# Optimization experiments

Measured on AMD Instinct MI355X. Metric: run time of the kernel, lower is better.

## Reference

```python
import jax, jax.numpy as jnp
import numpy as np

B, NQ, NK, D, H = 4, 512, 512, 128, 32  # batch, n_queries, n_keys, kq_size, mlp hidden


def setup_inputs() -> dict:
    key = jax.random.key(0)
    ks = jax.random.split(key, 7)
    s_in = 1.0 / np.sqrt(2 * D)
    s_h = 1.0 / np.sqrt(H)
    return {
        "keys": jax.random.normal(ks[0], (B, NK, D), dtype=jnp.float32),
        "queries": jax.random.normal(ks[1], (B, NQ, D), dtype=jnp.float32),
        # first MLP layer Linear(2D, H) split into key-half and query-half
        "Wk": jax.random.uniform(ks[2], (D, H), jnp.float32, -s_in, s_in),
        "Wq": jax.random.uniform(ks[3], (D, H), jnp.float32, -s_in, s_in),
        "b1": jax.random.uniform(ks[4], (H,), jnp.float32, -s_in, s_in),
        # second MLP layer Linear(H, 1)
        "w2": jax.random.uniform(ks[5], (H,), jnp.float32, -s_h, s_h),
        "b2": jax.random.uniform(ks[6], (), jnp.float32, -s_h, s_h),
    }


def reference(keys, queries, Wk, Wq, b1, w2, b2):
    # AdditiveScorer: logits[b,q,k] = w2 . tanh(W1 @ [keys[b,k]; queries[b,q]] + b1) + b2
    # Split the concat-linear into two GEMMs (identical math, no [B,Q,K,2D] tensor).
    kh = jnp.einsum("bkd,dh->bkh", keys, Wk)            # (B, NK, H)
    qh = jnp.einsum("bqd,dh->bqh", queries, Wq)          # (B, NQ, H)
    h = jnp.tanh(qh[:, :, None, :] + kh[:, None, :, :] + b1)  # (B, NQ, NK, H)
    logits = jnp.einsum("bqkh,h->bqk", h, w2) + b2       # (B, NQ, NK)
    attn = jax.nn.softmax(logits, axis=-1)               # softmax over keys
    context = jnp.einsum("bqk,bkd->bqd", attn, keys)     # weighted value sum (values = keys)
    return context
```

## Files before the change

### kernel.cpp

```cpp
#include <hip/hip_runtime.h>

#define B 4
#define NQ 512
#define NK 512
#define D 128
#define H 32
#define G 4
#define PS 2.8853900817779268f

__device__ __forceinline__ float rcp_f(float x)  { return __builtin_amdgcn_rcpf(x); }
__device__ __forceinline__ float exp2_f(float x) { return __builtin_amdgcn_exp2f(x); }

__device__ __forceinline__ void fma4(float4& a, const float4& v, float s) {
    a.x = fmaf(s, v.x, a.x);
    a.y = fmaf(s, v.y, a.y);
    a.z = fmaf(s, v.z, a.z);
    a.w = fmaf(s, v.w, a.w);
}

__global__ __launch_bounds__(256) void proj_kernel(
    const float* __restrict__ keys, const float* __restrict__ queries,
    const float* __restrict__ Wk, const float* __restrict__ Wq,
    const float* __restrict__ b1,
    float* __restrict__ Ek, float* __restrict__ eq)
{
    __shared__ float xs[8][D];
    const int tid = threadIdx.x;
    const int r0 = blockIdx.x * 8;
    const bool is_q = (r0 >= B * NK);
    const float* __restrict__ X = is_q ? (queries + (size_t)(r0 - B * NK) * D)
                                       : (keys + (size_t)r0 * D);
    const float* __restrict__ W = is_q ? Wq : Wk;

    reinterpret_cast<float4*>(&xs[0][0])[tid] =
        reinterpret_cast<const float4*>(X)[tid];
    __syncthreads();

    const int lr = tid >> 5;
    const int h  = tid & 31;
    float a0 = 0.f, a1 = 0.f, a2 = 0.f, a3 = 0.f;
    const float4* x4 = reinterpret_cast<const float4*>(&xs[lr][0]);
    #pragma unroll
    for (int i = 0; i < D / 4; ++i) {
        float4 v = x4[i];
        a0 = fmaf(v.x, W[(4 * i + 0) * H + h], a0);
        a1 = fmaf(v.y, W[(4 * i + 1) * H + h], a1);
        a2 = fmaf(v.z, W[(4 * i + 2) * H + h], a2);
        a3 = fmaf(v.w, W[(4 * i + 3) * H + h], a3);
    }
    float acc = (a0 + a1) + (a2 + a3);
    if (is_q) {
        const int rq = r0 - B * NK + lr;
        eq[(size_t)rq * H + h] = exp2_f(acc * PS);
    } else {
        const int r = r0 + lr;
        const int b = r >> 9;
        const int k = r & (NK - 1);
        Ek[((size_t)b * H + h) * NK + k] = exp2_f((acc + b1[h]) * PS);
    }
}

__global__ __launch_bounds__(512) void attend_kernel(
    const float* __restrict__ keys,
    const float* __restrict__ Ek,
    const float* __restrict__ eq,
    const float* __restrict__ w2,
    float* __restrict__ outp)
{
    __shared__ float lp[8][256];
    __shared__ float ex_t[G][NK];
    __shared__ float acc_s[16][G][D];
    __shared__ float eq_s[G][H];
    __shared__ float w2_s[H];

    const int tid  = threadIdx.x;
    const int lane = tid & 63;
    const int w    = tid >> 6;
    const int qw   = w & 3;
    const int half = w >> 2;
    const int b    = blockIdx.x >> 7;
    const int q0   = (blockIdx.x & 127) * G;

    if (lane < H) {
        if (w < 4)  eq_s[w][lane] = eq[((size_t)b * NQ + q0 + w) * H + lane];
        if (w == 4) w2_s[lane] = -PS * w2[lane];
    }
    __syncthreads();

    float l0 = 0.f, l1 = 0.f, l2 = 0.f, l3 = 0.f;
    const float* Ekb = Ek + (size_t)b * H * NK + half * 256;
    #pragma unroll 8
    for (int h = 0; h < H; ++h) {
        const float4 v = reinterpret_cast<const float4*>(Ekb + h * NK)[lane];
        const float ev = eq_s[qw][h];
        const float wp = w2_s[h];
        l0 = fmaf(wp, rcp_f(fmaf(ev, v.x, 1.f)), l0);
        l1 = fmaf(wp, rcp_f(fmaf(ev, v.y, 1.f)), l1);
        l2 = fmaf(wp, rcp_f(fmaf(ev, v.z, 1.f)), l2);
        l3 = fmaf(wp, rcp_f(fmaf(ev, v.w, 1.f)), l3);
    }
    {
        const float4 st = { l0, l1, l2, l3 };
        reinterpret_cast<float4*>(&lp[w][0])[lane] = st;
    }
    __syncthreads();

    if (w < 4) {
        float l[8];
        {
            const float4 L0 = reinterpret_cast<const float4*>(&lp[w][0])[lane];
            const float4 L1 = reinterpret_cast<const float4*>(&lp[w + 4][0])[lane];
            l[0] = L0.x; l[1] = L0.y; l[2] = L0.z; l[3] = L0.w;
            l[4] = L1.x; l[5] = L1.y; l[6] = L1.z; l[7] = L1.w;
        }
        float m = l[0];
        #pragma unroll
        for (int j = 1; j < 8; ++j) m = fmaxf(m, l[j]);
        #pragma unroll
        for (int off = 32; off; off >>= 1) m = fmaxf(m, __shfl_xor(m, off));
        float e[8], s = 0.f;
        #pragma unroll
        for (int j = 0; j < 8; ++j) { e[j] = exp2_f(l[j] - m); s += e[j]; }
        #pragma unroll
        for (int off = 32; off; off >>= 1) s += __shfl_xor(s, off);
        const float inv = 1.f / s;
        const float4 st0 = { e[0] * inv, e[1] * inv, e[2] * inv, e[3] * inv };
        const float4 st1 = { e[4] * inv, e[5] * inv, e[6] * inv, e[7] * inv };
        reinterpret_cast<float4*>(&ex_t[w][0])[lane]   = st0;
        reinterpret_cast<float4*>(&ex_t[w][256])[lane] = st1;
    }
    __syncthreads();

    const int dg = tid & 31;
    const int kp = tid >> 5;
    const float4* k4 = reinterpret_cast<const float4*>(
        keys + ((size_t)b * NK + kp * 32) * D) + dg;
    const float4* e0p = reinterpret_cast<const float4*>(&ex_t[0][kp * 32]);
    const float4* e1p = reinterpret_cast<const float4*>(&ex_t[1][kp * 32]);
    const float4* e2p = reinterpret_cast<const float4*>(&ex_t[2][kp * 32]);
    const float4* e3p = reinterpret_cast<const float4*>(&ex_t[3][kp * 32]);
    float4 a0 = {0,0,0,0}, a1 = a0, a2 = a0, a3 = a0;
    #pragma unroll 2
    for (int kk4 = 0; kk4 < 8; ++kk4) {
        float ea[4], eb[4], ec[4], ed[4];
        *reinterpret_cast<float4*>(ea) = e0p[kk4];
        *reinterpret_cast<float4*>(eb) = e1p[kk4];
        *reinterpret_cast<float4*>(ec) = e2p[kk4];
        *reinterpret_cast<float4*>(ed) = e3p[kk4];
        #pragma unroll
        for (int j = 0; j < 4; ++j) {
            float4 kv = k4[(size_t)(4 * kk4 + j) * (D / 4)];
            fma4(a0, kv, ea[j]);
            fma4(a1, kv, eb[j]);
            fma4(a2, kv, ec[j]);
            fma4(a3, kv, ed[j]);
        }
    }
    *reinterpret_cast<float4*>(&acc_s[kp][0][4 * dg]) = a0;
    *reinterpret_cast<float4*>(&acc_s[kp][1][4 * dg]) = a1;
    *reinterpret_cast<float4*>(&acc_s[kp][2][4 * dg]) = a2;
    *reinterpret_cast<float4*>(&acc_s[kp][3][4 * dg]) = a3;
    __syncthreads();

    const int g = tid >> 7;
    const int d = tid & 127;
    float r = 0.f;
    #pragma unroll
    for (int p = 0; p < 16; ++p) r += acc_s[p][g][d];
    outp[((size_t)b * NQ + q0 + g) * D + d] = r;
}

extern "C" void kernel_launch(void* const* d_in, const int* in_sizes, int n_in,
                              void* d_out, int out_size, void* d_ws, size_t ws_size,
                              hipStream_t stream) {
    const float* keys    = (const float*)d_in[0];
    const float* queries = (const float*)d_in[1];
    const float* Wk      = (const float*)d_in[2];
    const float* Wq      = (const float*)d_in[3];
    const float* b1      = (const float*)d_in[4];
    const float* w2      = (const float*)d_in[5];
    float* out = (float*)d_out;

    float* Ek = (float*)d_ws;
    float* eq = Ek + (size_t)B * H * NK;

    const int proj_blocks = (B * NK + B * NQ) / 8;
    proj_kernel<<<proj_blocks, 256, 0, stream>>>(keys, queries, Wk, Wq, b1, Ek, eq);
    attend_kernel<<<B * NQ / G, 512, 0, stream>>>(keys, Ek, eq, w2, out);
}
```

Baseline: 20.24 us.

## Process eight queries per block with LDS-staged key projections and packed FMA

The attend kernel now handles eight queries per block instead of four, so each block stages the batch's full exp-key projection slab (64KB) in LDS once and reuses it across all eight query waves. Each wave now scores a single query over all 512 keys, which removes the cross-wave logit merge and the max subtraction in the softmax. The scoring loop uses v_pk_fma_f32 on packed pairs. The value-sum phase keeps eight accumulators per thread, which doubles reuse of each loaded key. In exchange there are half as many blocks, much more LDS per block (about 82KB dynamic), higher register pressure, and a softmax without max subtraction that depends on logits staying bounded.

```diff
diff --git a/kernel.cpp b/kernel.cpp
--- a/kernel.cpp
+++ b/kernel.cpp
@@ -5,11 +5,19 @@
 #define NK 512
 #define D 128
 #define H 32
-#define G 4
+#define G 8
 #define PS 2.8853900817779268f
+
+typedef float f32x2 __attribute__((ext_vector_type(2)));
 
 __device__ __forceinline__ float rcp_f(float x)  { return __builtin_amdgcn_rcpf(x); }
 __device__ __forceinline__ float exp2_f(float x) { return __builtin_amdgcn_exp2f(x); }
+
+__device__ __forceinline__ f32x2 pk_fma(f32x2 a, f32x2 b, f32x2 c) {
+    f32x2 d;
+    asm("v_pk_fma_f32 %0, %1, %2, %3" : "=v"(d) : "v"(a), "v"(b), "v"(c));
+    return d;
+}
 
 __device__ __forceinline__ void fma4(float4& a, const float4& v, float s) {
     a.x = fmaf(s, v.x, a.x);
@@ -67,107 +75,128 @@
     const float* __restrict__ w2,
     float* __restrict__ outp)
 {
-    __shared__ float lp[8][256];
-    __shared__ float ex_t[G][NK];
-    __shared__ float acc_s[16][G][D];
-    __shared__ float eq_s[G][H];
-    __shared__ float w2_s[H];
+    extern __shared__ float smem[];
+    float* slab = smem;
+    float* exw  = smem + H * NK;
+    float* eqw  = smem + H * NK + G * NK;
 
     const int tid  = threadIdx.x;
     const int lane = tid & 63;
     const int w    = tid >> 6;
-    const int qw   = w & 3;
-    const int half = w >> 2;
-    const int b    = blockIdx.x >> 7;
-    const int q0   = (blockIdx.x & 127) * G;
-
-    if (lane < H) {
-        if (w < 4)  eq_s[w][lane] = eq[((size_t)b * NQ + q0 + w) * H + lane];
-        if (w == 4) w2_s[lane] = -PS * w2[lane];
-    }
-    __syncthreads();
-
-    float l0 = 0.f, l1 = 0.f, l2 = 0.f, l3 = 0.f;
-    const float* Ekb = Ek + (size_t)b * H * NK + half * 256;
-    #pragma unroll 8
+    const int b    = blockIdx.x >> 6;
+    const int q0   = (blockIdx.x & 63) * G;
+
+    {
+        const float4* src = reinterpret_cast<const float4*>(Ek + (size_t)b * H * NK);
+        float4* dst = reinterpret_cast<float4*>(slab);
+        #pragma unroll
+        for (int i = 0; i < 8; ++i)
+            dst[tid + 512 * i] = src[tid + 512 * i];
+    }
+    if (tid < G * H) {
+        const int g = tid >> 5, h = tid & 31;
+        const float ev = eq[((size_t)b * NQ + q0 + g) * H + h];
+        const float wp = -PS * w2[h];
+        reinterpret_cast<float4*>(eqw)[tid] = float4{ev, ev, wp, wp};
+    }
+    __syncthreads();
+
+    f32x2 acc0 = {0.f, 0.f}, acc1 = acc0, acc2 = acc0, acc3 = acc0;
+    const f32x2 one2 = {1.f, 1.f};
+    const float4* eqw4 = reinterpret_cast<const float4*>(eqw) + w * H;
+    #pragma unroll 4
     for (int h = 0; h < H; ++h) {
-        const float4 v = reinterpret_cast<const float4*>(Ekb + h * NK)[lane];
-        const float ev = eq_s[qw][h];
-        const float wp = w2_s[h];
-        l0 = fmaf(wp, rcp_f(fmaf(ev, v.x, 1.f)), l0);
-        l1 = fmaf(wp, rcp_f(fmaf(ev, v.y, 1.f)), l1);
-        l2 = fmaf(wp, rcp_f(fmaf(ev, v.z, 1.f)), l2);
-        l3 = fmaf(wp, rcp_f(fmaf(ev, v.w, 1.f)), l3);
-    }
-    {
-        const float4 st = { l0, l1, l2, l3 };
-        reinterpret_cast<float4*>(&lp[w][0])[lane] = st;
-    }
-    __syncthreads();
-
-    if (w < 4) {
-        float l[8];
-        {
-            const float4 L0 = reinterpret_cast<const float4*>(&lp[w][0])[lane];
-            const float4 L1 = reinterpret_cast<const float4*>(&lp[w + 4][0])[lane];
-            l[0] = L0.x; l[1] = L0.y; l[2] = L0.z; l[3] = L0.w;
-            l[4] = L1.x; l[5] = L1.y; l[6] = L1.z; l[7] = L1.w;
-        }
-        float m = l[0];
-        #pragma unroll
-        for (int j = 1; j < 8; ++j) m = fmaxf(m, l[j]);
-        #pragma unroll
-        for (int off = 32; off; off >>= 1) m = fmaxf(m, __shfl_xor(m, off));
-        float e[8], s = 0.f;
-        #pragma unroll
-        for (int j = 0; j < 8; ++j) { e[j] = exp2_f(l[j] - m); s += e[j]; }
-        #pragma unroll
-        for (int off = 32; off; off >>= 1) s += __shfl_xor(s, off);
-        const float inv = 1.f / s;
-        const float4 st0 = { e[0] * inv, e[1] * inv, e[2] * inv, e[3] * inv };
-        const float4 st1 = { e[4] * inv, e[5] * inv, e[6] * inv, e[7] * inv };
-        reinterpret_cast<float4*>(&ex_t[w][0])[lane]   = st0;
-        reinterpret_cast<float4*>(&ex_t[w][256])[lane] = st1;
-    }
+        const float4 ew = eqw4[h];
+        const f32x2 ev2 = {ew.x, ew.y};
+        const f32x2 wp2 = {ew.z, ew.w};
+        const float4 v0 = reinterpret_cast<const float4*>(slab + h * NK)[lane];
+        const float4 v1 = reinterpret_cast<const float4*>(slab + h * NK + 256)[lane];
+        f32x2 u;
+        u = pk_fma(ev2, f32x2{v0.x, v0.y}, one2);
+        u.x = rcp_f(u.x); u.y = rcp_f(u.y);
+        acc0 = pk_fma(wp2, u, acc0);
+        u = pk_fma(ev2, f32x2{v0.z, v0.w}, one2);
+        u.x = rcp_f(u.x); u.y = rcp_f(u.y);
+        acc1 = pk_fma(wp2, u, acc1);
+        u = pk_fma(ev2, f32x2{v1.x, v1.y}, one2);
+        u.x = rcp_f(u.x); u.y = rcp_f(u.y);
+        acc2 = pk_fma(wp2, u, acc2);
+        u = pk_fma(ev2, f32x2{v1.z, v1.w}, one2);
+        u.x = rcp_f(u.x); u.y = rcp_f(u.y);
+        acc3 = pk_fma(wp2, u, acc3);
+    }
+
+    float e[8];
+    e[0] = exp2_f(acc0.x); e[1] = exp2_f(acc0.y);
+    e[2] = exp2_f(acc1.x); e[3] = exp2_f(acc1.y);
+    e[4] = exp2_f(acc2.x); e[5] = exp2_f(acc2.y);
+    e[6] = exp2_f(acc3.x); e[7] = exp2_f(acc3.y);
+    float s = ((e[0] + e[1]) + (e[2] + e[3])) + ((e[4] + e[5]) + (e[6] + e[7]));
+    #pragma unroll
+    for (int off = 32; off; off >>= 1) s += __shfl_xor(s, off);
+    const float inv = 1.f / s;
+    reinterpret_cast<float4*>(exw + w * NK)[lane] =
+        float4{e[0] * inv, e[1] * inv, e[2] * inv, e[3] * inv};
+    reinterpret_cast<float4*>(exw + w * NK + 256)[lane] =
+        float4{e[4] * inv, e[5] * inv, e[6] * inv, e[7] * inv};
     __syncthreads();
 
     const int dg = tid & 31;
     const int kp = tid >> 5;
     const float4* k4 = reinterpret_cast<const float4*>(
         keys + ((size_t)b * NK + kp * 32) * D) + dg;
-    const float4* e0p = reinterpret_cast<const float4*>(&ex_t[0][kp * 32]);
-    const float4* e1p = reinterpret_cast<const float4*>(&ex_t[1][kp * 32]);
-    const float4* e2p = reinterpret_cast<const float4*>(&ex_t[2][kp * 32]);
-    const float4* e3p = reinterpret_cast<const float4*>(&ex_t[3][kp * 32]);
-    float4 a0 = {0,0,0,0}, a1 = a0, a2 = a0, a3 = a0;
+    float4 a0 = {0,0,0,0}, a1 = a0, a2 = a0, a3 = a0, a4 = a0, a5 = a0, a6 = a0, a7 = a0;
     #pragma unroll 2
     for (int kk4 = 0; kk4 < 8; ++kk4) {
-        float ea[4], eb[4], ec[4], ed[4];
-        *reinterpret_cast<float4*>(ea) = e0p[kk4];
-        *reinterpret_cast<float4*>(eb) = e1p[kk4];
-        *reinterpret_cast<float4*>(ec) = e2p[kk4];
-        *reinterpret_cast<float4*>(ed) = e3p[kk4];
+        float4 eg0, eg1, eg2, eg3, eg4, eg5, eg6, eg7;
+        eg0 = reinterpret_cast<const float4*>(exw + 0 * NK + kp * 32)[kk4];
+        eg1 = reinterpret_cast<const float4*>(exw + 1 * NK + kp * 32)[kk4];
+        eg2 = reinterpret_cast<const float4*>(exw + 2 * NK + kp * 32)[kk4];
+        eg3 = reinterpret_cast<const float4*>(exw + 3 * NK + kp * 32)[kk4];
+        eg4 = reinterpret_cast<const float4*>(exw + 4 * NK + kp * 32)[kk4];
+        eg5 = reinterpret_cast<const float4*>(exw + 5 * NK + kp * 32)[kk4];
+        eg6 = reinterpret_cast<const float4*>(exw + 6 * NK + kp * 32)[kk4];
+        eg7 = reinterpret_cast<const float4*>(exw + 7 * NK + kp * 32)[kk4];
         #pragma unroll
         for (int j = 0; j < 4; ++j) {
-            float4 kv = k4[(size_t)(4 * kk4 + j) * (D / 4)];
-            fma4(a0, kv, ea[j]);
-            fma4(a1, kv, eb[j]);
-            fma4(a2, kv, ec[j]);
-            fma4(a3, kv, ed[j]);
+            const float4 kv = k4[(size_t)(4 * kk4 + j) * (D / 4)];
+            const float s0 = j == 0 ? eg0.x : j == 1 ? eg0.y : j == 2 ? eg0.z : eg0.w;
+            const float s1 = j == 0 ? eg1.x : j == 1 ? eg1.y : j == 2 ? eg1.z : eg1.w;
+            const float s2 = j == 0 ? eg2.x : j == 1 ? eg2.y : j == 2 ? eg2.z : eg2.w;
+            const float s3 = j == 0 ? eg3.x : j == 1 ? eg3.y : j == 2 ? eg3.z : eg3.w;
+            const float s4 = j == 0 ? eg4.x : j == 1 ? eg4.y : j == 2 ? eg4.z : eg4.w;
+            const float s5 = j == 0 ? eg5.x : j == 1 ? eg5.y : j == 2 ? eg5.z : eg5.w;
+            const float s6 = j == 0 ? eg6.x : j == 1 ? eg6.y : j == 2 ? eg6.z : eg6.w;
+            const float s7 = j == 0 ? eg7.x : j == 1 ? eg7.y : j == 2 ? eg7.z : eg7.w;
+            fma4(a0, kv, s0); fma4(a1, kv, s1); fma4(a2, kv, s2); fma4(a3, kv, s3);
+            fma4(a4, kv, s4); fma4(a5, kv, s5); fma4(a6, kv, s6); fma4(a7, kv, s7);
         }
     }
-    *reinterpret_cast<float4*>(&acc_s[kp][0][4 * dg]) = a0;
-    *reinterpret_cast<float4*>(&acc_s[kp][1][4 * dg]) = a1;
-    *reinterpret_cast<float4*>(&acc_s[kp][2][4 * dg]) = a2;
-    *reinterpret_cast<float4*>(&acc_s[kp][3][4 * dg]) = a3;
-    __syncthreads();
-
-    const int g = tid >> 7;
-    const int d = tid & 127;
-    float r = 0.f;
+    {
+        float* accm = slab;
+        const int base = (kp * G) * D + 4 * dg;
+        *reinterpret_cast<float4*>(accm + base + 0 * D) = a0;
+        *reinterpret_cast<float4*>(accm + base + 1 * D) = a1;
+        *reinterpret_cast<float4*>(accm + base + 2 * D) = a2;
+        *reinterpret_cast<float4*>(accm + base + 3 * D) = a3;
+        *reinterpret_cast<float4*>(accm + base + 4 * D) = a4;
+        *reinterpret_cast<float4*>(accm + base + 5 * D) = a5;
+        *reinterpret_cast<float4*>(accm + base + 6 * D) = a6;
+        *reinterpret_cast<float4*>(accm + base + 7 * D) = a7;
+    }
+    __syncthreads();
+
+    const float* accm = slab;
     #pragma unroll
-    for (int p = 0; p < 16; ++p) r += acc_s[p][g][d];
-    outp[((size_t)b * NQ + q0 + g) * D + d] = r;
+    for (int r0 = 0; r0 < 2; ++r0) {
+        const int o = tid + r0 * 512;
+        const int g = o >> 7;
+        const int d = o & 127;
+        float r = 0.f;
+        #pragma unroll
+        for (int p = 0; p < 16; ++p) r += accm[(p * G + g) * D + d];
+        outp[((size_t)b * NQ + q0 + g) * D + d] = r;
+    }
 }
 
 extern "C" void kernel_launch(void* const* d_in, const int* in_sizes, int n_in,
@@ -186,5 +215,7 @@
 
     const int proj_blocks = (B * NK + B * NQ) / 8;
     proj_kernel<<<proj_blocks, 256, 0, stream>>>(keys, queries, Wk, Wq, b1, Ek, eq);
-    attend_kernel<<<B * NQ / G, 512, 0, stream>>>(keys, Ek, eq, w2, out);
-}
+
+    const size_t lds_bytes = (size_t)(H * NK + G * NK + G * H * 4) * sizeof(float);
+    attend_kernel<<<B * NQ / G, 512, lds_bytes, stream>>>(keys, Ek, eq, w2, out);
+}
```

After: 20.13 us. About the same (-0.6%).

## Compute logits one key per thread for all four queries; drop softmax max pass

Applied to the files above, without the earlier changes.

The logit phase is remapped so each of the 512 threads owns one key and computes its logit for all four queries. Each Ek value is now loaded once and reused across queries, and eq and w2 become wave-uniform global loads instead of shared-memory staging. The softmax max-subtraction is dropped, since the logits are bounded by the sum of |w2| (tanh is bounded). The row sum is done with a shuffle reduction plus a small shared array, which removes one barrier and the partial-logit shared buffer. The probabilities are stored as [NK][G] so the AV loop reads one float4 per key, giving a different shared-memory access pattern.

```diff
diff --git a/kernel.cpp b/kernel.cpp
--- a/kernel.cpp
+++ b/kernel.cpp
@@ -67,106 +67,82 @@
     const float* __restrict__ w2,
     float* __restrict__ outp)
 {
-    __shared__ float lp[8][256];
-    __shared__ float ex_t[G][NK];
-    __shared__ float acc_s[16][G][D];
-    __shared__ float eq_s[G][H];
-    __shared__ float w2_s[H];
+    __shared__ float exw[NK][G];
+    __shared__ float red[8][G];
+    __shared__ float accm[16][G][D];
 
-    const int tid  = threadIdx.x;
-    const int lane = tid & 63;
-    const int w    = tid >> 6;
-    const int qw   = w & 3;
-    const int half = w >> 2;
-    const int b    = blockIdx.x >> 7;
-    const int q0   = (blockIdx.x & 127) * G;
+    const int tid = threadIdx.x;
+    const int b   = blockIdx.x >> 7;
+    const int q0  = (blockIdx.x & 127) * G;
 
-    if (lane < H) {
-        if (w < 4)  eq_s[w][lane] = eq[((size_t)b * NQ + q0 + w) * H + lane];
-        if (w == 4) w2_s[lane] = -PS * w2[lane];
+    float acc0 = 0.f, acc1 = 0.f, acc2 = 0.f, acc3 = 0.f;
+    const float* Ekc = Ek + (size_t)b * H * NK + tid;
+    const float* eqb = eq + ((size_t)b * NQ + q0) * H;
+    #pragma unroll
+    for (int h = 0; h < H; ++h) {
+        const float ekv = Ekc[h * NK];
+        const float w2h = w2[h];
+        const float ev0 = eqb[0 * H + h];
+        const float ev1 = eqb[1 * H + h];
+        const float ev2 = eqb[2 * H + h];
+        const float ev3 = eqb[3 * H + h];
+        acc0 = fmaf(w2h, rcp_f(fmaf(ev0, ekv, 1.f)), acc0);
+        acc1 = fmaf(w2h, rcp_f(fmaf(ev1, ekv, 1.f)), acc1);
+        acc2 = fmaf(w2h, rcp_f(fmaf(ev2, ekv, 1.f)), acc2);
+        acc3 = fmaf(w2h, rcp_f(fmaf(ev3, ekv, 1.f)), acc3);
     }
+    float e0 = exp2_f(-PS * acc0);
+    float e1 = exp2_f(-PS * acc1);
+    float e2 = exp2_f(-PS * acc2);
+    float e3 = exp2_f(-PS * acc3);
+
+    float s0 = e0, s1 = e1, s2 = e2, s3 = e3;
+    #pragma unroll
+    for (int off = 32; off; off >>= 1) {
+        s0 += __shfl_xor(s0, off);
+        s1 += __shfl_xor(s1, off);
+        s2 += __shfl_xor(s2, off);
+        s3 += __shfl_xor(s3, off);
+    }
+    if ((tid & 63) == 0)
+        *reinterpret_cast<float4*>(&red[tid >> 6][0]) = float4{s0, s1, s2, s3};
     __syncthreads();
-
-    float l0 = 0.f, l1 = 0.f, l2 = 0.f, l3 = 0.f;
-    const float* Ekb = Ek + (size_t)b * H * NK + half * 256;
-    #pragma unroll 8
-    for (int h = 0; h < H; ++h) {
-        const float4 v = reinterpret_cast<const float4*>(Ekb + h * NK)[lane];
-        const float ev = eq_s[qw][h];
-        const float wp = w2_s[h];
-        l0 = fmaf(wp, rcp_f(fmaf(ev, v.x, 1.f)), l0);
-        l1 = fmaf(wp, rcp_f(fmaf(ev, v.y, 1.f)), l1);
-        l2 = fmaf(wp, rcp_f(fmaf(ev, v.z, 1.f)), l2);
-        l3 = fmaf(wp, rcp_f(fmaf(ev, v.w, 1.f)), l3);
+    float4 sum = {0.f, 0.f, 0.f, 0.f};
+    #pragma unroll
+    for (int p = 0; p < 8; ++p) {
+        const float4 v = *reinterpret_cast<const float4*>(&red[p][0]);
+        sum.x += v.x; sum.y += v.y; sum.z += v.z; sum.w += v.w;
     }
-    {
-        const float4 st = { l0, l1, l2, l3 };
-        reinterpret_cast<float4*>(&lp[w][0])[lane] = st;
-    }
-    __syncthreads();
-
-    if (w < 4) {
-        float l[8];
-        {
-            const float4 L0 = reinterpret_cast<const float4*>(&lp[w][0])[lane];
-            const float4 L1 = reinterpret_cast<const float4*>(&lp[w + 4][0])[lane];
-            l[0] = L0.x; l[1] = L0.y; l[2] = L0.z; l[3] = L0.w;
-            l[4] = L1.x; l[5] = L1.y; l[6] = L1.z; l[7] = L1.w;
-        }
-        float m = l[0];
-        #pragma unroll
-        for (int j = 1; j < 8; ++j) m = fmaxf(m, l[j]);
-        #pragma unroll
-        for (int off = 32; off; off >>= 1) m = fmaxf(m, __shfl_xor(m, off));
-        float e[8], s = 0.f;
-        #pragma unroll
-        for (int j = 0; j < 8; ++j) { e[j] = exp2_f(l[j] - m); s += e[j]; }
-        #pragma unroll
-        for (int off = 32; off; off >>= 1) s += __shfl_xor(s, off);
-        const float inv = 1.f / s;
-        const float4 st0 = { e[0] * inv, e[1] * inv, e[2] * inv, e[3] * inv };
-        const float4 st1 = { e[4] * inv, e[5] * inv, e[6] * inv, e[7] * inv };
-        reinterpret_cast<float4*>(&ex_t[w][0])[lane]   = st0;
-        reinterpret_cast<float4*>(&ex_t[w][256])[lane] = st1;
-    }
+    *reinterpret_cast<float4*>(&exw[tid][0]) =
+        float4{e0 * rcp_f(sum.x), e1 * rcp_f(sum.y),
+               e2 * rcp_f(sum.z), e3 * rcp_f(sum.w)};
     __syncthreads();
 
     const int dg = tid & 31;
     const int kp = tid >> 5;
     const float4* k4 = reinterpret_cast<const float4*>(
         keys + ((size_t)b * NK + kp * 32) * D) + dg;
-    const float4* e0p = reinterpret_cast<const float4*>(&ex_t[0][kp * 32]);
-    const float4* e1p = reinterpret_cast<const float4*>(&ex_t[1][kp * 32]);
-    const float4* e2p = reinterpret_cast<const float4*>(&ex_t[2][kp * 32]);
-    const float4* e3p = reinterpret_cast<const float4*>(&ex_t[3][kp * 32]);
     float4 a0 = {0,0,0,0}, a1 = a0, a2 = a0, a3 = a0;
-    #pragma unroll 2
-    for (int kk4 = 0; kk4 < 8; ++kk4) {
-        float ea[4], eb[4], ec[4], ed[4];
-        *reinterpret_cast<float4*>(ea) = e0p[kk4];
-        *reinterpret_cast<float4*>(eb) = e1p[kk4];
-        *reinterpret_cast<float4*>(ec) = e2p[kk4];
-        *reinterpret_cast<float4*>(ed) = e3p[kk4];
-        #pragma unroll
-        for (int j = 0; j < 4; ++j) {
-            float4 kv = k4[(size_t)(4 * kk4 + j) * (D / 4)];
-            fma4(a0, kv, ea[j]);
-            fma4(a1, kv, eb[j]);
-            fma4(a2, kv, ec[j]);
-            fma4(a3, kv, ed[j]);
-        }
+    #pragma unroll 4
+    for (int kk = 0; kk < 32; ++kk) {
+        const float4 ev = *reinterpret_cast<const float4*>(&exw[kp * 32 + kk][0]);
+        const float4 kv = k4[(size_t)kk * (D / 4)];
+        fma4(a0, kv, ev.x);
+        fma4(a1, kv, ev.y);
+        fma4(a2, kv, ev.z);
+        fma4(a3, kv, ev.w);
     }
-    *reinterpret_cast<float4*>(&acc_s[kp][0][4 * dg]) = a0;
-    *reinterpret_cast<float4*>(&acc_s[kp][1][4 * dg]) = a1;
-    *reinterpret_cast<float4*>(&acc_s[kp][2][4 * dg]) = a2;
-    *reinterpret_cast<float4*>(&acc_s[kp][3][4 * dg]) = a3;
+    *reinterpret_cast<float4*>(&accm[kp][0][4 * dg]) = a0;
+    *reinterpret_cast<float4*>(&accm[kp][1][4 * dg]) = a1;
+    *reinterpret_cast<float4*>(&accm[kp][2][4 * dg]) = a2;
+    *reinterpret_cast<float4*>(&accm[kp][3][4 * dg]) = a3;
     __syncthreads();
 
     const int g = tid >> 7;
     const int d = tid & 127;
     float r = 0.f;
     #pragma unroll
-    for (int p = 0; p < 16; ++p) r += acc_s[p][g][d];
+    for (int p = 0; p < 16; ++p) r += accm[p][g][d];
     outp[((size_t)b * NQ + q0 + g) * D + d] = r;
 }
 
```

New measurement: 20.48 us. Within noise of the previous version (+1.2%).
